# Performance work log

Hardware: AMD Instinct MI355X
Metric: run time of the kernel (lower is better)

## Reference

```python
import jax, jax.numpy as jnp
import numpy as np

D_K = 16  # fixed by module globals
N_HEADS = 1

def setup_inputs() -> dict:
    key = jax.random.key(0)
    ks = jax.random.split(key, 7)
    B, H, S, d = 4, N_HEADS, 4096, D_K
    Q = jax.random.normal(ks[0], (B, H, S, d), dtype=jnp.float32)
    K = jax.random.normal(ks[1], (B, H, S, d), dtype=jnp.float32)
    V = jax.random.normal(ks[2], (B, H, S, d), dtype=jnp.float32)
    attn_mask = jax.random.randint(ks[3], (B, H, S, S), 0, 2).astype(jnp.bool_)
    link_sim_mat = jax.random.uniform(ks[4], (B, S, S), dtype=jnp.float32)
    # 1x1 Conv2d(1->1) params: a single scalar weight and scalar bias
    sim_w = jax.random.normal(ks[5], (), dtype=jnp.float32) * 0.5
    sim_b = jax.random.normal(ks[6], (), dtype=jnp.float32) * 0.1
    return {"Q": Q, "K": K, "V": V, "attn_mask": attn_mask,
            "link_sim_mat": link_sim_mat, "sim_w": sim_w, "sim_b": sim_b}

def reference(Q, K, V, attn_mask, link_sim_mat, sim_w, sim_b):
    # scores = QK^T / sqrt(d_k)  -> [B,H,S,S]
    scores = jnp.einsum('bhqd,bhkd->bhqk', Q, K) / jnp.sqrt(jnp.float32(D_K))
    # 1x1 conv on [B,1,S,S] with 1 in/out channel == scalar affine
    sim_link = sim_w * link_sim_mat + sim_b          # [B,S,S]
    scores = scores + sim_link[:, None, :, :]        # broadcast over heads
    scores = jnp.where(attn_mask, jnp.float32(-1e9), scores)
    attn = jax.nn.softmax(scores, axis=-1)
    context = jnp.einsum('bhqk,bhkd->bhqd', attn, V)
    return (context, attn)
```

## Files before the change

### kernel.cpp

```cpp
#include <hip/hip_runtime.h>

#define SS    4096
#define DK    16
#define NB    4
#define TQ    4
#define BLOCK 256
#define KPT   16

__global__ void detect_mask_dtype(const unsigned* __restrict__ m,
                                  int* __restrict__ flag)
{
    unsigned acc = 0;
    for (int i = 0; i < 1024; ++i) acc |= m[i];
    *flag = (acc > 1u) ? 1 : 0;
}

__global__ __launch_bounds__(BLOCK)
void attn_fused(const float* __restrict__ Qm, const float* __restrict__ Km,
                const float* __restrict__ Vm, const void*  __restrict__ Mraw,
                const float* __restrict__ Lm, const float* __restrict__ WP,
                const float* __restrict__ BP, const int*   __restrict__ flagp,
                float* __restrict__ Co, float* __restrict__ Ao)
{
    __shared__ float redl[4][TQ];
    __shared__ float redc[4][TQ][DK];

    const int tid = threadIdx.x;
    const int b   = blockIdx.x >> 10;
    const int q0  = (blockIdx.x & 1023) * TQ;

    const bool  m8 = (*flagp != 0);
    const float sw = WP[0];
    const float sb = BP[0];

    const float* qp = Qm + ((size_t)b * SS + q0) * DK;
    const float* kp = Km + (size_t)b * SS * DK;
    const float* vp = Vm + (size_t)b * SS * DK;
    const size_t mrow = (size_t)b * SS * SS + (size_t)q0 * SS;
    const int*           mp32 = (const int*)Mraw           + mrow;
    const unsigned char* mp8  = (const unsigned char*)Mraw + mrow;
    const float* lp = Lm + mrow;
    float*       ap = Ao + mrow;

    float qreg[TQ][DK];
    #pragma unroll
    for (int qq = 0; qq < TQ; ++qq)
        #pragma unroll
        for (int d = 0; d < DK; ++d)
            qreg[qq][d] = __uint_as_float(
                __builtin_amdgcn_readfirstlane(__float_as_uint(qp[qq * DK + d])));

    const int k0 = tid * KPT;

    float p[TQ][KPT];
    float lsum[TQ] = {0.f, 0.f, 0.f, 0.f};

    #pragma unroll
    for (int j = 0; j < KPT / 4; ++j) {
        int4     mi[TQ];
        unsigned mu[TQ];
        float4   li[TQ];
        if (m8) {
            #pragma unroll
            for (int qq = 0; qq < TQ; ++qq)
                mu[qq] = *(const unsigned*)(mp8 + (size_t)qq * SS + k0 + 4 * j);
        } else {
            #pragma unroll
            for (int qq = 0; qq < TQ; ++qq)
                mi[qq] = *(const int4*)(mp32 + (size_t)qq * SS + k0 + 4 * j);
        }
        #pragma unroll
        for (int qq = 0; qq < TQ; ++qq)
            li[qq] = *(const float4*)(lp + (size_t)qq * SS + k0 + 4 * j);

        #pragma unroll
        for (int u = 0; u < 4; ++u) {
            const int i = 4 * j + u;
            const int k = k0 + i;
            const float4 ka = *(const float4*)(kp + (size_t)k * DK + 0);
            const float4 kb = *(const float4*)(kp + (size_t)k * DK + 4);
            const float4 kc = *(const float4*)(kp + (size_t)k * DK + 8);
            const float4 kd = *(const float4*)(kp + (size_t)k * DK + 12);
            const float kr[DK] = {ka.x, ka.y, ka.z, ka.w,
                                  kb.x, kb.y, kb.z, kb.w,
                                  kc.x, kc.y, kc.z, kc.w,
                                  kd.x, kd.y, kd.z, kd.w};
            #pragma unroll
            for (int qq = 0; qq < TQ; ++qq) {
                float s = 0.f;
                #pragma unroll
                for (int d = 0; d < DK; ++d)
                    s = fmaf(qreg[qq][d], kr[d], s);
                const float lv = (u == 0) ? li[qq].x : (u == 1) ? li[qq].y
                                : (u == 2) ? li[qq].z : li[qq].w;
                const int mv = m8
                    ? (int)((mu[qq] >> (8 * u)) & 0xffu)
                    : ((u == 0) ? mi[qq].x : (u == 1) ? mi[qq].y
                     : (u == 2) ? mi[qq].z : mi[qq].w);
                s = s * 0.25f + fmaf(sw, lv, sb);
                const float e  = __expf(s);
                const float pv = mv ? 0.f : e;
                p[qq][i] = pv;
                lsum[qq] += pv;
            }
        }
    }

    const int lane = tid & 63;
    const int wv   = tid >> 6;
    #pragma unroll
    for (int qq = 0; qq < TQ; ++qq) {
        float v = lsum[qq];
        #pragma unroll
        for (int off = 32; off; off >>= 1)
            v += __shfl_down(v, off);
        lsum[qq] = v;
    }
    if (lane == 0) {
        #pragma unroll
        for (int qq = 0; qq < TQ; ++qq)
            redl[wv][qq] = lsum[qq];
    }
    __syncthreads();
    float rl[TQ];
    #pragma unroll
    for (int qq = 0; qq < TQ; ++qq)
        rl[qq] = 1.0f / (redl[0][qq] + redl[1][qq] + redl[2][qq] + redl[3][qq]);

    float ctx[TQ][DK];
    #pragma unroll
    for (int qq = 0; qq < TQ; ++qq)
        #pragma unroll
        for (int d = 0; d < DK; ++d)
            ctx[qq][d] = 0.f;

    #pragma unroll
    for (int i = 0; i < KPT; ++i) {
        const int k = k0 + i;
        const float4 va = *(const float4*)(vp + (size_t)k * DK + 0);
        const float4 vb = *(const float4*)(vp + (size_t)k * DK + 4);
        const float4 vc = *(const float4*)(vp + (size_t)k * DK + 8);
        const float4 vd = *(const float4*)(vp + (size_t)k * DK + 12);
        const float vr[DK] = {va.x, va.y, va.z, va.w,
                              vb.x, vb.y, vb.z, vb.w,
                              vc.x, vc.y, vc.z, vc.w,
                              vd.x, vd.y, vd.z, vd.w};
        #pragma unroll
        for (int qq = 0; qq < TQ; ++qq) {
            const float pn = p[qq][i] * rl[qq];
            p[qq][i] = pn;
            #pragma unroll
            for (int d = 0; d < DK; ++d)
                ctx[qq][d] = fmaf(pn, vr[d], ctx[qq][d]);
        }
    }

    #pragma unroll
    for (int qq = 0; qq < TQ; ++qq)
        #pragma unroll
        for (int j = 0; j < KPT / 4; ++j) {
            float4 st = {p[qq][4 * j + 0], p[qq][4 * j + 1],
                         p[qq][4 * j + 2], p[qq][4 * j + 3]};
            *(float4*)(ap + (size_t)qq * SS + k0 + 4 * j) = st;
        }

    #pragma unroll
    for (int qq = 0; qq < TQ; ++qq)
        #pragma unroll
        for (int d = 0; d < DK; ++d) {
            float v = ctx[qq][d];
            #pragma unroll
            for (int off = 32; off; off >>= 1)
                v += __shfl_down(v, off);
            ctx[qq][d] = v;
        }
    if (lane == 0) {
        #pragma unroll
        for (int qq = 0; qq < TQ; ++qq)
            #pragma unroll
            for (int d = 0; d < DK; ++d)
                redc[wv][qq][d] = ctx[qq][d];
    }
    __syncthreads();
    if (tid < TQ * DK) {
        const int qq = tid >> 4;
        const int d  = tid & 15;
        const float v = redc[0][qq][d] + redc[1][qq][d]
                      + redc[2][qq][d] + redc[3][qq][d];
        Co[((size_t)b * SS + q0 + qq) * DK + d] = v;
    }
}

extern "C" void kernel_launch(void* const* d_in, const int* in_sizes, int n_in,
                              void* d_out, int out_size, void* d_ws, size_t ws_size,
                              hipStream_t stream)
{
    (void)in_sizes; (void)n_in; (void)ws_size; (void)out_size;

    const float* Q  = (const float*)d_in[0];
    const float* K  = (const float*)d_in[1];
    const float* V  = (const float*)d_in[2];
    const void*  M  = d_in[3];
    const float* L  = (const float*)d_in[4];
    const float* W  = (const float*)d_in[5];
    const float* Bp = (const float*)d_in[6];

    int* flag = (int*)d_ws;

    float* Co = (float*)d_out;
    float* Ao = (float*)d_out + (size_t)NB * SS * DK;

    detect_mask_dtype<<<1, 1, 0, stream>>>((const unsigned*)M, flag);

    dim3 grid(NB * SS / TQ);
    dim3 block(BLOCK);
    attn_fused<<<grid, block, 0, stream>>>(Q, K, V, M, L, W, Bp, flag, Co, Ao);
}
```

Before: 1.018 ms.

## Coalesce mask/link/attn accesses, halve rows per block, use nontemporal streaming

Each thread now handles interleaved 4-wide chunks (j*BLOCK+tid)*4, so a wavefront's mask, link and attn accesses are contiguous instead of 64-byte strided per thread. The block covers 2 query rows instead of 4, doubling the grid and cutting register use, and launch bounds ask for 4 blocks per CU. The streamed mask, link and attn traffic uses nontemporal loads and stores so it does not pollute the cache. In exchange, K and V rows are reloaded across twice as many blocks.

```diff
diff --git a/kernel.cpp b/kernel.cpp
--- a/kernel.cpp
+++ b/kernel.cpp
@@ -3,9 +3,12 @@
 #define SS    4096
 #define DK    16
 #define NB    4
-#define TQ    4
+#define TQ    2
 #define BLOCK 256
-#define KPT   16
+#define NJ    4
+
+typedef float fx4 __attribute__((ext_vector_type(4)));
+typedef int   ix4 __attribute__((ext_vector_type(4)));
 
 __global__ void detect_mask_dtype(const unsigned* __restrict__ m,
                                   int* __restrict__ flag)
@@ -15,7 +18,7 @@
     *flag = (acc > 1u) ? 1 : 0;
 }
 
-__global__ __launch_bounds__(BLOCK)
+__global__ __launch_bounds__(BLOCK, 4)
 void attn_fused(const float* __restrict__ Qm, const float* __restrict__ Km,
                 const float* __restrict__ Vm, const void*  __restrict__ Mraw,
                 const float* __restrict__ Lm, const float* __restrict__ WP,
@@ -26,8 +29,8 @@
     __shared__ float redc[4][TQ][DK];
 
     const int tid = threadIdx.x;
-    const int b   = blockIdx.x >> 10;
-    const int q0  = (blockIdx.x & 1023) * TQ;
+    const int b   = blockIdx.x >> 11;
+    const int q0  = (blockIdx.x & 2047) * TQ;
 
     const bool  m8 = (*flagp != 0);
     const float sw = WP[0];
@@ -50,47 +53,52 @@
             qreg[qq][d] = __uint_as_float(
                 __builtin_amdgcn_readfirstlane(__float_as_uint(qp[qq * DK + d])));
 
-    const int k0 = tid * KPT;
-
-    float p[TQ][KPT];
-    float lsum[TQ] = {0.f, 0.f, 0.f, 0.f};
-
-    #pragma unroll
-    for (int j = 0; j < KPT / 4; ++j) {
-        int4     mi[TQ];
+    float p[TQ][4 * NJ];
+    float lsum[TQ] = {0.f, 0.f};
+
+    #pragma unroll
+    for (int j = 0; j < NJ; ++j) {
+        const int c = (j * BLOCK + tid) * 4;
+
         unsigned mu[TQ];
-        float4   li[TQ];
+        ix4      mi[TQ];
+        fx4      li[TQ];
         if (m8) {
             #pragma unroll
             for (int qq = 0; qq < TQ; ++qq)
-                mu[qq] = *(const unsigned*)(mp8 + (size_t)qq * SS + k0 + 4 * j);
+                mu[qq] = __builtin_nontemporal_load(
+                             (const unsigned*)(mp8 + (size_t)qq * SS + c));
         } else {
             #pragma unroll
             for (int qq = 0; qq < TQ; ++qq)
-                mi[qq] = *(const int4*)(mp32 + (size_t)qq * SS + k0 + 4 * j);
+                mi[qq] = __builtin_nontemporal_load(
+                             (const ix4*)(mp32 + (size_t)qq * SS + c));
         }
         #pragma unroll
         for (int qq = 0; qq < TQ; ++qq)
-            li[qq] = *(const float4*)(lp + (size_t)qq * SS + k0 + 4 * j);
+            li[qq] = __builtin_nontemporal_load(
+                         (const fx4*)(lp + (size_t)qq * SS + c));
 
         #pragma unroll
         for (int u = 0; u < 4; ++u) {
-            const int i = 4 * j + u;
-            const int k = k0 + i;
-            const float4 ka = *(const float4*)(kp + (size_t)k * DK + 0);
-            const float4 kb = *(const float4*)(kp + (size_t)k * DK + 4);
-            const float4 kc = *(const float4*)(kp + (size_t)k * DK + 8);
-            const float4 kd = *(const float4*)(kp + (size_t)k * DK + 12);
-            const float kr[DK] = {ka.x, ka.y, ka.z, ka.w,
-                                  kb.x, kb.y, kb.z, kb.w,
-                                  kc.x, kc.y, kc.z, kc.w,
-                                  kd.x, kd.y, kd.z, kd.w};
+            const int k = c + u;
+            const fx4 ka = *(const fx4*)(kp + (size_t)k * DK + 0);
+            const fx4 kb = *(const fx4*)(kp + (size_t)k * DK + 4);
+            const fx4 kc = *(const fx4*)(kp + (size_t)k * DK + 8);
+            const fx4 kd = *(const fx4*)(kp + (size_t)k * DK + 12);
             #pragma unroll
             for (int qq = 0; qq < TQ; ++qq) {
-                float s = 0.f;
-                #pragma unroll
-                for (int d = 0; d < DK; ++d)
-                    s = fmaf(qreg[qq][d], kr[d], s);
+                const float* q = qreg[qq];
+                float s;
+                s = fmaf(q[0],  ka.x, 0.f);
+                s = fmaf(q[1],  ka.y, s);  s = fmaf(q[2],  ka.z, s);
+                s = fmaf(q[3],  ka.w, s);  s = fmaf(q[4],  kb.x, s);
+                s = fmaf(q[5],  kb.y, s);  s = fmaf(q[6],  kb.z, s);
+                s = fmaf(q[7],  kb.w, s);  s = fmaf(q[8],  kc.x, s);
+                s = fmaf(q[9],  kc.y, s);  s = fmaf(q[10], kc.z, s);
+                s = fmaf(q[11], kc.w, s);  s = fmaf(q[12], kd.x, s);
+                s = fmaf(q[13], kd.y, s);  s = fmaf(q[14], kd.z, s);
+                s = fmaf(q[15], kd.w, s);
                 const float lv = (u == 0) ? li[qq].x : (u == 1) ? li[qq].y
                                 : (u == 2) ? li[qq].z : li[qq].w;
                 const int mv = m8
@@ -100,7 +108,7 @@
                 s = s * 0.25f + fmaf(sw, lv, sb);
                 const float e  = __expf(s);
                 const float pv = mv ? 0.f : e;
-                p[qq][i] = pv;
+                p[qq][4 * j + u] = pv;
                 lsum[qq] += pv;
             }
         }
@@ -135,34 +143,45 @@
             ctx[qq][d] = 0.f;
 
     #pragma unroll
-    for (int i = 0; i < KPT; ++i) {
-        const int k = k0 + i;
-        const float4 va = *(const float4*)(vp + (size_t)k * DK + 0);
-        const float4 vb = *(const float4*)(vp + (size_t)k * DK + 4);
-        const float4 vc = *(const float4*)(vp + (size_t)k * DK + 8);
-        const float4 vd = *(const float4*)(vp + (size_t)k * DK + 12);
-        const float vr[DK] = {va.x, va.y, va.z, va.w,
-                              vb.x, vb.y, vb.z, vb.w,
-                              vc.x, vc.y, vc.z, vc.w,
-                              vd.x, vd.y, vd.z, vd.w};
+    for (int j = 0; j < NJ; ++j) {
+        const int c = (j * BLOCK + tid) * 4;
+        #pragma unroll
+        for (int u = 0; u < 4; ++u) {
+            const int k = c + u;
+            const fx4 va = *(const fx4*)(vp + (size_t)k * DK + 0);
+            const fx4 vb = *(const fx4*)(vp + (size_t)k * DK + 4);
+            const fx4 vc = *(const fx4*)(vp + (size_t)k * DK + 8);
+            const fx4 vd = *(const fx4*)(vp + (size_t)k * DK + 12);
+            #pragma unroll
+            for (int qq = 0; qq < TQ; ++qq) {
+                const float pn = p[qq][4 * j + u] * rl[qq];
+                p[qq][4 * j + u] = pn;
+                ctx[qq][0]  = fmaf(pn, va.x, ctx[qq][0]);
+                ctx[qq][1]  = fmaf(pn, va.y, ctx[qq][1]);
+                ctx[qq][2]  = fmaf(pn, va.z, ctx[qq][2]);
+                ctx[qq][3]  = fmaf(pn, va.w, ctx[qq][3]);
+                ctx[qq][4]  = fmaf(pn, vb.x, ctx[qq][4]);
+                ctx[qq][5]  = fmaf(pn, vb.y, ctx[qq][5]);
+                ctx[qq][6]  = fmaf(pn, vb.z, ctx[qq][6]);
+                ctx[qq][7]  = fmaf(pn, vb.w, ctx[qq][7]);
+                ctx[qq][8]  = fmaf(pn, vc.x, ctx[qq][8]);
+                ctx[qq][9]  = fmaf(pn, vc.y, ctx[qq][9]);
+                ctx[qq][10] = fmaf(pn, vc.z, ctx[qq][10]);
+                ctx[qq][11] = fmaf(pn, vc.w, ctx[qq][11]);
+                ctx[qq][12] = fmaf(pn, vd.x, ctx[qq][12]);
+                ctx[qq][13] = fmaf(pn, vd.y, ctx[qq][13]);
+                ctx[qq][14] = fmaf(pn, vd.z, ctx[qq][14]);
+                ctx[qq][15] = fmaf(pn, vd.w, ctx[qq][15]);
+            }
+        }
         #pragma unroll
         for (int qq = 0; qq < TQ; ++qq) {
-            const float pn = p[qq][i] * rl[qq];
-            p[qq][i] = pn;
-            #pragma unroll
-            for (int d = 0; d < DK; ++d)
-                ctx[qq][d] = fmaf(pn, vr[d], ctx[qq][d]);
-        }
-    }
-
-    #pragma unroll
-    for (int qq = 0; qq < TQ; ++qq)
-        #pragma unroll
-        for (int j = 0; j < KPT / 4; ++j) {
-            float4 st = {p[qq][4 * j + 0], p[qq][4 * j + 1],
-                         p[qq][4 * j + 2], p[qq][4 * j + 3]};
-            *(float4*)(ap + (size_t)qq * SS + k0 + 4 * j) = st;
-        }
+            fx4 st = {p[qq][4 * j + 0], p[qq][4 * j + 1],
+                      p[qq][4 * j + 2], p[qq][4 * j + 3]};
+            __builtin_nontemporal_store(st,
+                (fx4*)(ap + (size_t)qq * SS + c));
+        }
+    }
 
     #pragma unroll
     for (int qq = 0; qq < TQ; ++qq)
```

New measurement: 1.695 ms. 66.4% more time.
